# Kernel tuning notes

Measured on AMD Instinct MI355X. Metric: run time of the kernel, lower is better.

The kernel has to match this reference:

```python
import jax, jax.numpy as jnp
import numpy as np

N = 100_000      # nodes
E = 1_600_000    # edges (avg degree 16)
B = 50           # graphs in batch
GSIZE = N // B   # nodes per graph
IN = 128
HID = 128
NC = 10
K = 2


def setup_inputs() -> dict:
    key = jax.random.key(0)
    ks = jax.random.split(key, 10)
    # edges kept within each graph so the batched readout is realistic
    g = jax.random.randint(ks[0], (E,), 0, B)
    src = (g * GSIZE + jax.random.randint(ks[1], (E,), 0, GSIZE)).astype(jnp.int32)
    dst = (g * GSIZE + jax.random.randint(ks[2], (E,), 0, GSIZE)).astype(jnp.int32)
    graph_ids = (jnp.arange(N) // GSIZE).astype(jnp.int32)
    x = jax.random.normal(ks[3], (N, IN), jnp.float32)
    s1 = 1.0 / np.sqrt(K * IN)
    s2 = 1.0 / np.sqrt(K * HID)
    sc = 1.0 / np.sqrt(HID)
    W1 = jax.random.normal(ks[4], (K * IN, HID), jnp.float32) * s1
    b1 = jnp.zeros((HID,), jnp.float32)
    W2 = jax.random.normal(ks[5], (K * HID, HID), jnp.float32) * s2
    b2 = jnp.zeros((HID,), jnp.float32)
    Wc = jax.random.normal(ks[6], (HID, NC), jnp.float32) * sc
    bc = jnp.zeros((NC,), jnp.float32)
    return dict(x=x, W1=W1, b1=b1, W2=W2, b2=b2, Wc=Wc, bc=bc,
                src=src, dst=dst, graph_ids=graph_ids)


def _spmm_norm(feat, src, dst, dinv):
    # D^{-1/2} A D^{-1/2} feat  (copy_u + sum over in-edges)
    m = (feat * dinv)[src]                                    # [E, D]
    agg = jax.ops.segment_sum(m, dst, num_segments=N)         # [N, D]
    return agg * dinv


def _cheb_conv(feat, src, dst, dinv, W, b):
    # lambda_max = 2 -> re_norm = 1, L_hat = -D^{-1/2} A D^{-1/2}
    Tx0 = feat
    Tx1 = -_spmm_norm(feat, src, dst, dinv)                   # k=2 Cheb recursion
    h = jnp.concatenate([Tx0, Tx1], axis=-1) @ W + b          # DGL Linear(k*in, out)
    return jax.nn.relu(h)


def reference(x, W1, b1, W2, b2, Wc, bc, src, dst, graph_ids):
    deg = jax.ops.segment_sum(jnp.ones((E,), jnp.float32), dst, num_segments=N)
    dinv = jnp.clip(deg, 1.0, None) ** -0.5                   # in-degree^{-1/2}
    dinv = dinv[:, None]
    h = _cheb_conv(x, src, dst, dinv, W1, b1)                 # [N, HID]
    h = _cheb_conv(h, src, dst, dinv, W2, b2)                 # [N, HID]
    hg = jax.ops.segment_max(h, graph_ids, num_segments=B)    # MaxPooling readout [B, HID]
    return hg @ Wc + bc                                       # [B, NC]
```

## Files before the change

kernel.cpp:

```cpp
#include <hip/hip_runtime.h>

#define N_NODES 100000
#define N_EDGES 1600000
#define NB      50
#define GSIZE   2000
#define FEAT    128
#define NC      10
#define NSB     400
#define BCAP    5120
#define CHUNK   2048
#define NBLK_A  782

using short8 = __attribute__((ext_vector_type(8))) short;
using f32x4  = __attribute__((ext_vector_type(4))) float;

__device__ __forceinline__ unsigned bf16rnd(float f) {
    unsigned u = __float_as_uint(f);
    return (u + 0x7fffu + ((u >> 16) & 1u)) >> 16;
}
__device__ __forceinline__ float blo(unsigned w) { return __uint_as_float(w << 16); }
__device__ __forceinline__ float bhi(unsigned w) { return __uint_as_float(w & 0xffff0000u); }

__device__ __forceinline__ void gload_lds16(const void* g, void* l) {
    __builtin_amdgcn_global_load_lds(
        (const __attribute__((address_space(1))) unsigned int*)g,
        (__attribute__((address_space(3))) unsigned int*)l, 16, 0, 0);
}

__device__ __forceinline__ int graph_of(int k, int gi) {
    if (gi < 6) return k + 8 * gi;
    return (k < 2) ? (48 + k) : -1;
}

__global__ __launch_bounds__(256) void k_binA(
    const int* __restrict__ src, const int* __restrict__ dst,
    unsigned* __restrict__ gbuf, int* __restrict__ gcur) {
    __shared__ int cnt[NSB];
    __shared__ int base[NSB];
    __shared__ int gbase[NSB];
    __shared__ int tsum[256];
    __shared__ unsigned stage[CHUNK];
    __shared__ unsigned short bslot[CHUNK];
    __shared__ int total_s;
    int tid = threadIdx.x;
    int e0 = blockIdx.x * CHUNK;
    for (int i = tid; i < NSB; i += 256) cnt[i] = 0;
    __syncthreads();

    unsigned pv[8]; int pb[8], pr[8];
#pragma unroll
    for (int q = 0; q < 8; ++q) {
        int e = e0 + q * 256 + tid;
        pb[q] = -1;
        if (e < N_EDGES) {
            int d = dst[e];
            int g = d / 2000;
            int l = d - g * 2000;
            int sb = g * 8 + l / 250;
            pv[q] = ((unsigned)src[e] << 11) | (unsigned)l;
            pb[q] = sb;
            pr[q] = atomicAdd(&cnt[sb], 1);
        }
    }
    __syncthreads();
    int v0 = (2 * tid     < NSB) ? cnt[2 * tid]     : 0;
    int v1 = (2 * tid + 1 < NSB) ? cnt[2 * tid + 1] : 0;
    int loc = v0 + v1;
    tsum[tid] = loc; __syncthreads();
    for (int off = 1; off < 256; off <<= 1) {
        int t = (tid >= off) ? tsum[tid - off] : 0;
        __syncthreads(); tsum[tid] += t; __syncthreads();
    }
    int pref = tsum[tid] - loc;
    if (2 * tid     < NSB) base[2 * tid]     = pref;
    if (2 * tid + 1 < NSB) base[2 * tid + 1] = pref + v0;
    if (tid == 255) total_s = tsum[255];
    __syncthreads();
#pragma unroll
    for (int q = 0; q < 8; ++q) {
        if (pb[q] >= 0) {
            int s = base[pb[q]] + pr[q];
            stage[s] = pv[q];
            bslot[s] = (unsigned short)pb[q];
        }
    }
    for (int b = tid; b < NSB; b += 256) gbase[b] = atomicAdd(&gcur[b], cnt[b]);
    __syncthreads();
    int total = total_s;
    for (int s = tid; s < total; s += 256) {
        int b = bslot[s];
        gbuf[(size_t)b * BCAP + gbase[b] + (s - base[b])] = stage[s];
    }
}

__global__ __launch_bounds__(256) void k_prepB(
    const unsigned* __restrict__ gbuf, const int* __restrict__ gcur,
    int* __restrict__ rowstart, float* __restrict__ dinv, float* __restrict__ sdeg,
    int* __restrict__ csrc) {
    __shared__ int hist[256];
    __shared__ int tsum[256];
    __shared__ int lcur[256];
    __shared__ int stage[BCAP];
    __shared__ int base_s;
    int B = blockIdx.x; int k = B & 7, j = B >> 3;
    int gi = j >> 3, q = j & 7;
    int g = graph_of(k, gi);
    if (g < 0) return;
    int tid = threadIdx.x;
    int sb = g * 8 + q;
    int n0l = q * 250;
    hist[tid] = 0;
    int acc = 0;
    for (int i = tid; i < sb; i += 256) acc += gcur[i];
    tsum[tid] = acc;
    __syncthreads();
    for (int off = 128; off > 0; off >>= 1) {
        if (tid < off) tsum[tid] += tsum[tid + off];
        __syncthreads();
    }
    if (tid == 0) base_s = tsum[0];
    int nq = gcur[sb];
    const unsigned* bp = gbuf + (size_t)sb * BCAP;
    for (int i = tid; i < nq; i += 256)
        atomicAdd(&hist[(int)(bp[i] & 2047u) - n0l], 1);
    __syncthreads();
    int base = base_s;
    int v = hist[tid];
    tsum[tid] = v; __syncthreads();
    for (int off = 1; off < 256; off <<= 1) {
        int t = (tid >= off) ? tsum[tid - off] : 0;
        __syncthreads(); tsum[tid] += t; __syncthreads();
    }
    int pref = tsum[tid] - v;
    lcur[tid] = pref;
    if (tid < 250) {
        int node = g * GSIZE + n0l + tid;
        rowstart[node] = base + pref;
        float d = fmaxf((float)v, 1.f);
        dinv[node] = rsqrtf(d);
        sdeg[node] = sqrtf(d);
    }
    if (g == 49 && q == 7 && tid == 0) rowstart[N_NODES] = base + nq;
    __syncthreads();
    for (int i = tid; i < nq; i += 256) {
        unsigned w = bp[i];
        int d = (int)(w & 2047u) - n0l;
        int p = atomicAdd(&lcur[d], 1);
        stage[p] = (int)(w >> 11);
    }
    __syncthreads();
    for (int s = tid; s < nq; s += 256)
        csrc[base + s] = stage[s];
}

__global__ __launch_bounds__(256) void k_convert(const float* __restrict__ x,
                          const float* __restrict__ dinv, ushort* __restrict__ Yh) {
    int B = blockIdx.x; int k = B & 7, j = B >> 3;
    int gi = j / 250, local = j % 250;
    int g = graph_of(k, gi);
    if (g < 0) return;
    int tid = threadIdx.x;
    int r = tid >> 5, c = tid & 31;
    int node = g * GSIZE + local * 8 + r;
    float dv = dinv[node];
    float4 v = ((const float4*)x)[node * 32 + c];
    uint2 yo;
    yo.x = bf16rnd(v.x * dv) | (bf16rnd(v.y * dv) << 16);
    yo.y = bf16rnd(v.z * dv) | (bf16rnd(v.w * dv) << 16);
    ((uint2*)Yh)[node * 32 + c] = yo;
}

__global__ void k_packW(const float* __restrict__ W1, const float* __restrict__ W2,
                        ushort* __restrict__ W1h, ushort* __restrict__ W1l,
                        ushort* __restrict__ W2h, ushort* __restrict__ W2l) {
    int b = blockIdx.x;
    const float* W = (b < 128) ? W1 : W2;
    ushort* Wh = (b < 128) ? W1h : W2h;
    ushort* Wl = (b < 128) ? W1l : W2l;
    int idx = (b & 127) * 256 + threadIdx.x;
    int j = idx & 7, l = (idx >> 3) & 63, kb = (idx >> 9) & 7, c = idx >> 12;
    int k = kb * 32 + (l >> 4) * 8 + j;
    int col = c * 16 + (l & 15);
    float w = W[k * 128 + col];
    unsigned h = bf16rnd(w);
    float rem = w - __uint_as_float(h << 16);
    Wh[idx] = (ushort)h;
    Wl[idx] = (ushort)bf16rnd(rem);
}

__device__ __forceinline__ void acc8(float* a, uint4 u) {
    a[0] += blo(u.x); a[1] += bhi(u.x); a[2] += blo(u.y); a[3] += bhi(u.y);
    a[4] += blo(u.z); a[5] += bhi(u.z); a[6] += blo(u.w); a[7] += bhi(u.w);
}
__global__ __launch_bounds__(256) void k_gather(
    const ushort* __restrict__ Yh, const float* __restrict__ dinv,
    const int* __restrict__ rowstart, const int* __restrict__ csrc,
    ushort* __restrict__ Th) {
    int B = blockIdx.x; int k = B & 7, j = B >> 3;
    int gi = j / 125, local = j % 125;
    int g = graph_of(k, gi);
    if (g < 0) return;
    int tid = threadIdx.x;
    int c = tid & 15;
    int i = tid >> 4;
    int n = g * GSIZE + local * 16 + i;
    int rs = rowstart[n], re = rowstart[n + 1];
    const uint4* Y4 = (const uint4*)Yh;
    float a0[8] = {0.f}, a1[8] = {0.f}, a2[8] = {0.f}, a3[8] = {0.f};
    int e = rs;
    for (; e + 3 < re; e += 4) {
        int s0 = csrc[e], s1 = csrc[e + 1], s2 = csrc[e + 2], s3 = csrc[e + 3];
        uint4 u0 = Y4[s0 * 16 + c];
        uint4 u1 = Y4[s1 * 16 + c];
        uint4 u2 = Y4[s2 * 16 + c];
        uint4 u3 = Y4[s3 * 16 + c];
        acc8(a0, u0); acc8(a1, u1); acc8(a2, u2); acc8(a3, u3);
    }
    for (; e < re; ++e) {
        uint4 u = Y4[csrc[e] * 16 + c];
        acc8(a0, u);
    }
#pragma unroll
    for (int t = 0; t < 8; ++t) a0[t] = (a0[t] + a1[t]) + (a2[t] + a3[t]);
    float dn = -dinv[n];
    uint4 o;
    o.x = bf16rnd(a0[0] * dn) | (bf16rnd(a0[1] * dn) << 16);
    o.y = bf16rnd(a0[2] * dn) | (bf16rnd(a0[3] * dn) << 16);
    o.z = bf16rnd(a0[4] * dn) | (bf16rnd(a0[5] * dn) << 16);
    o.w = bf16rnd(a0[6] * dn) | (bf16rnd(a0[7] * dn) << 16);
    ((uint4*)Th)[n * 16 + c] = o;
}

__global__ __launch_bounds__(256, 4) void k_gemm(
    const ushort* __restrict__ Yh, const ushort* __restrict__ Th,
    const ushort* __restrict__ Wh, const ushort* __restrict__ Wl,
    const float* __restrict__ bias, const float* __restrict__ dinv,
    const float* __restrict__ sdeg,
    ushort* __restrict__ Oy, float* __restrict__ hg, int mode) {
    __shared__ uint4 ldsY[1280];
    __shared__ uint4 ldsT[1280];
    int B = blockIdx.x; int k = B & 7, j = B >> 3;
    int gi = j / 25, local = j % 25;
    int g = graph_of(k, gi);
    if (g < 0) return;
    int tid = threadIdx.x;
    int lane = tid & 63, wave = tid >> 6;
    int m = lane & 15, quad = lane >> 4;
    int rowbase = g * GSIZE + local * 80;

    const uint4* Y4 = (const uint4*)Yh;
    const uint4* T4 = (const uint4*)Th;
#pragma unroll
    for (int it = 0; it < 5; ++it) {
        int ci = it * 256 + tid;
        int lr = ci >> 4, cc = ci & 15;
        int sc = cc ^ (lr & 7);
        size_t go = (size_t)(rowbase + lr) * 16 + sc;
        uint4* ly = &ldsY[it * 256 + wave * 64];
        uint4* lt = &ldsT[it * 256 + wave * 64];
        gload_lds16(Y4 + go, ly);
        gload_lds16(T4 + go, lt);
    }
    __syncthreads();

#pragma unroll 1
    for (int ci2 = 0; ci2 < 2; ++ci2) {
        int c = wave + ci2 * 4;
        int colc = c * 16 + m;
        short8 wh[8], wl[8];
#pragma unroll
        for (int kb = 0; kb < 8; ++kb) {
            int bo = ((c * 8 + kb) * 64 + lane) * 8;
            wh[kb] = *reinterpret_cast<const short8*>(Wh + bo);
            wl[kb] = *reinterpret_cast<const short8*>(Wl + bo);
        }
#pragma unroll
        for (int kb = 0; kb < 8; ++kb) {
            asm volatile("" : "+v"(wh[kb]), "+v"(wl[kb]));
        }
        float bb = bias[colc];
        float runc = 0.f;

#pragma unroll 1
        for (int rt = 0; rt < 5; ++rt) {
            int wrow = rowbase + rt * 16;
            int lr = rt * 16 + m;
            f32x4 aA = {0.f, 0.f, 0.f, 0.f}, aB = {0.f, 0.f, 0.f, 0.f};
#pragma unroll
            for (int kb = 0; kb < 4; ++kb) {
                int qq = (kb * 4 + quad) ^ (m & 7);
                short8 aY = *reinterpret_cast<const short8*>(&ldsY[(lr << 4) | qq]);
                short8 aT = *reinterpret_cast<const short8*>(&ldsT[(lr << 4) | qq]);
                aA = __builtin_amdgcn_mfma_f32_16x16x32_bf16(aY, wh[kb],     aA, 0, 0, 0);
                aA = __builtin_amdgcn_mfma_f32_16x16x32_bf16(aY, wl[kb],     aA, 0, 0, 0);
                aB = __builtin_amdgcn_mfma_f32_16x16x32_bf16(aT, wh[kb + 4], aB, 0, 0, 0);
                aB = __builtin_amdgcn_mfma_f32_16x16x32_bf16(aT, wl[kb + 4], aB, 0, 0, 0);
            }
            if (mode == 0) {
#pragma unroll
                for (int r = 0; r < 4; ++r) {
                    int orow = wrow + quad * 4 + r;
                    float s = sdeg[orow], dv = dinv[orow];
                    float v = fmaxf(aA[r] * s + aB[r] + bb, 0.f);
                    Oy[orow * FEAT + colc] = (ushort)bf16rnd(v * dv);
                }
            } else {
#pragma unroll
                for (int r = 0; r < 4; ++r) {
                    float s = sdeg[wrow + quad * 4 + r];
                    runc = fmaxf(runc, fmaxf(aA[r] * s + aB[r] + bb, 0.f));
                }
            }
        }
        if (mode == 1) {
            runc = fmaxf(runc, __shfl_xor(runc, 16));
            runc = fmaxf(runc, __shfl_xor(runc, 32));
            if (lane < 16) {
                atomicMax((int*)&hg[g * FEAT + colc], __float_as_int(runc));
            }
        }
    }
}

__global__ void k_classify(const float* __restrict__ hg, const float* __restrict__ Wc,
                           const float* __restrict__ bc, float* __restrict__ out) {
    int g = blockIdx.x, t = threadIdx.x;
    if (t < NC) {
        float acc = bc[t];
        for (int j = 0; j < FEAT; ++j) acc += hg[g * FEAT + j] * Wc[j * NC + t];
        out[g * NC + t] = acc;
    }
}

extern "C" void kernel_launch(void* const* d_in, const int* in_sizes, int n_in,
                              void* d_out, int out_size, void* d_ws, size_t ws_size,
                              hipStream_t stream) {
    const float* x   = (const float*)d_in[0];
    const float* W1  = (const float*)d_in[1];
    const float* b1  = (const float*)d_in[2];
    const float* W2  = (const float*)d_in[3];
    const float* b2  = (const float*)d_in[4];
    const float* Wc  = (const float*)d_in[5];
    const float* bc  = (const float*)d_in[6];
    const int*   src = (const int*)d_in[7];
    const int*   dst = (const int*)d_in[8];
    float* out = (float*)d_out;

    char* ws = (char*)d_ws;
    size_t off = 0;
    auto alloc = [&](size_t bytes) { char* p = ws + off; off += (bytes + 255) & ~(size_t)255; return p; };
    int*      gcur     = (int*)     alloc(NSB * 4);
    float*    hg       = (float*)   alloc(NB * FEAT * 4);
    float*    dinv     = (float*)   alloc(N_NODES * 4);
    float*    sdeg     = (float*)   alloc(N_NODES * 4);
    int*      rowstart = (int*)     alloc((N_NODES + 1) * 4);
    unsigned* gbuf     = (unsigned*)alloc((size_t)NSB * BCAP * 4);
    int*      csrc     = (int*)     alloc((size_t)N_EDGES * 4);
    ushort*   W1h      = (ushort*)  alloc(256 * 128 * 2);
    ushort*   W1l      = (ushort*)  alloc(256 * 128 * 2);
    ushort*   W2h      = (ushort*)  alloc(256 * 128 * 2);
    ushort*   W2l      = (ushort*)  alloc(256 * 128 * 2);
    ushort*   Yh       = (ushort*)  alloc((size_t)N_NODES * FEAT * 2);
    ushort*   Y2h      = (ushort*)  alloc((size_t)N_NODES * FEAT * 2);
    ushort*   Th       = (ushort*)  alloc((size_t)N_NODES * FEAT * 2);

    hipMemsetAsync(gcur, 0, 1792 + NB * FEAT * 4, stream);

    k_binA<<<NBLK_A, 256, 0, stream>>>(src, dst, gbuf, gcur);
    k_prepB<<<448, 256, 0, stream>>>(gbuf, gcur, rowstart, dinv, sdeg, csrc);

    k_packW<<<256, 256, 0, stream>>>(W1, W2, W1h, W1l, W2h, W2l);
    k_convert<<<14000, 256, 0, stream>>>(x, dinv, Yh);

    k_gather<<<7000, 256, 0, stream>>>(Yh, dinv, rowstart, csrc, Th);
    k_gemm<<<1400, 256, 0, stream>>>(Yh, Th, W1h, W1l, b1, dinv, sdeg, Y2h, nullptr, 0);
    k_gather<<<7000, 256, 0, stream>>>(Y2h, dinv, rowstart, csrc, Th);
    k_gemm<<<1400, 256, 0, stream>>>(Y2h, Th, W2h, W2l, b2, dinv, sdeg, nullptr, hg, 1);

    k_classify<<<NB, 64, 0, stream>>>(hg, Wc, bc, out);
}
```

Baseline: 277.2 us.

## Fuse neighbor gather into GEMM kernel, keeping aggregated features in LDS

```diff
diff --git a/kernel.cpp b/kernel.cpp
--- a/kernel.cpp
+++ b/kernel.cpp
@@ -30,6 +30,11 @@
 __device__ __forceinline__ int graph_of(int k, int gi) {
     if (gi < 6) return k + 8 * gi;
     return (k < 2) ? (48 + k) : -1;
+}
+
+__device__ __forceinline__ void acc8(float* a, uint4 u) {
+    a[0] += blo(u.x); a[1] += bhi(u.x); a[2] += blo(u.y); a[3] += bhi(u.y);
+    a[4] += blo(u.z); a[5] += bhi(u.z); a[6] += blo(u.w); a[7] += bhi(u.w);
 }
 
 __global__ __launch_bounds__(256) void k_binA(
@@ -188,54 +193,12 @@
     Wl[idx] = (ushort)bf16rnd(rem);
 }
 
-__device__ __forceinline__ void acc8(float* a, uint4 u) {
-    a[0] += blo(u.x); a[1] += bhi(u.x); a[2] += blo(u.y); a[3] += bhi(u.y);
-    a[4] += blo(u.z); a[5] += bhi(u.z); a[6] += blo(u.w); a[7] += bhi(u.w);
-}
-__global__ __launch_bounds__(256) void k_gather(
-    const ushort* __restrict__ Yh, const float* __restrict__ dinv,
-    const int* __restrict__ rowstart, const int* __restrict__ csrc,
-    ushort* __restrict__ Th) {
-    int B = blockIdx.x; int k = B & 7, j = B >> 3;
-    int gi = j / 125, local = j % 125;
-    int g = graph_of(k, gi);
-    if (g < 0) return;
-    int tid = threadIdx.x;
-    int c = tid & 15;
-    int i = tid >> 4;
-    int n = g * GSIZE + local * 16 + i;
-    int rs = rowstart[n], re = rowstart[n + 1];
-    const uint4* Y4 = (const uint4*)Yh;
-    float a0[8] = {0.f}, a1[8] = {0.f}, a2[8] = {0.f}, a3[8] = {0.f};
-    int e = rs;
-    for (; e + 3 < re; e += 4) {
-        int s0 = csrc[e], s1 = csrc[e + 1], s2 = csrc[e + 2], s3 = csrc[e + 3];
-        uint4 u0 = Y4[s0 * 16 + c];
-        uint4 u1 = Y4[s1 * 16 + c];
-        uint4 u2 = Y4[s2 * 16 + c];
-        uint4 u3 = Y4[s3 * 16 + c];
-        acc8(a0, u0); acc8(a1, u1); acc8(a2, u2); acc8(a3, u3);
-    }
-    for (; e < re; ++e) {
-        uint4 u = Y4[csrc[e] * 16 + c];
-        acc8(a0, u);
-    }
-#pragma unroll
-    for (int t = 0; t < 8; ++t) a0[t] = (a0[t] + a1[t]) + (a2[t] + a3[t]);
-    float dn = -dinv[n];
-    uint4 o;
-    o.x = bf16rnd(a0[0] * dn) | (bf16rnd(a0[1] * dn) << 16);
-    o.y = bf16rnd(a0[2] * dn) | (bf16rnd(a0[3] * dn) << 16);
-    o.z = bf16rnd(a0[4] * dn) | (bf16rnd(a0[5] * dn) << 16);
-    o.w = bf16rnd(a0[6] * dn) | (bf16rnd(a0[7] * dn) << 16);
-    ((uint4*)Th)[n * 16 + c] = o;
-}
-
-__global__ __launch_bounds__(256, 4) void k_gemm(
-    const ushort* __restrict__ Yh, const ushort* __restrict__ Th,
+__global__ __launch_bounds__(256, 4) void k_gg(
+    const ushort* __restrict__ Yh,
     const ushort* __restrict__ Wh, const ushort* __restrict__ Wl,
     const float* __restrict__ bias, const float* __restrict__ dinv,
     const float* __restrict__ sdeg,
+    const int* __restrict__ rowstart, const int* __restrict__ csrc,
     ushort* __restrict__ Oy, float* __restrict__ hg, int mode) {
     __shared__ uint4 ldsY[1280];
     __shared__ uint4 ldsT[1280];
@@ -249,17 +212,47 @@
     int rowbase = g * GSIZE + local * 80;
 
     const uint4* Y4 = (const uint4*)Yh;
-    const uint4* T4 = (const uint4*)Th;
 #pragma unroll
     for (int it = 0; it < 5; ++it) {
         int ci = it * 256 + tid;
         int lr = ci >> 4, cc = ci & 15;
         int sc = cc ^ (lr & 7);
         size_t go = (size_t)(rowbase + lr) * 16 + sc;
-        uint4* ly = &ldsY[it * 256 + wave * 64];
-        uint4* lt = &ldsT[it * 256 + wave * 64];
-        gload_lds16(Y4 + go, ly);
-        gload_lds16(T4 + go, lt);
+        gload_lds16(Y4 + go, &ldsY[it * 256 + wave * 64]);
+    }
+
+    {
+        int c = tid & 15;
+        int i = tid >> 4;
+#pragma unroll 1
+        for (int b = 0; b < 5; ++b) {
+            int lr = b * 16 + i;
+            int n = rowbase + lr;
+            int rs = rowstart[n], re = rowstart[n + 1];
+            float a0[8] = {0.f}, a1[8] = {0.f}, a2[8] = {0.f}, a3[8] = {0.f};
+            int e = rs;
+            for (; e + 3 < re; e += 4) {
+                int s0 = csrc[e], s1 = csrc[e + 1], s2 = csrc[e + 2], s3 = csrc[e + 3];
+                uint4 u0 = Y4[s0 * 16 + c];
+                uint4 u1 = Y4[s1 * 16 + c];
+                uint4 u2 = Y4[s2 * 16 + c];
+                uint4 u3 = Y4[s3 * 16 + c];
+                acc8(a0, u0); acc8(a1, u1); acc8(a2, u2); acc8(a3, u3);
+            }
+            for (; e < re; ++e) {
+                uint4 u = Y4[csrc[e] * 16 + c];
+                acc8(a0, u);
+            }
+#pragma unroll
+            for (int t = 0; t < 8; ++t) a0[t] = (a0[t] + a1[t]) + (a2[t] + a3[t]);
+            float dn = -dinv[n];
+            uint4 o;
+            o.x = bf16rnd(a0[0] * dn) | (bf16rnd(a0[1] * dn) << 16);
+            o.y = bf16rnd(a0[2] * dn) | (bf16rnd(a0[3] * dn) << 16);
+            o.z = bf16rnd(a0[4] * dn) | (bf16rnd(a0[5] * dn) << 16);
+            o.w = bf16rnd(a0[6] * dn) | (bf16rnd(a0[7] * dn) << 16);
+            ldsT[(lr << 4) | (c ^ (i & 7))] = o;
+        }
     }
     __syncthreads();
 
@@ -362,7 +355,6 @@
     ushort*   W2l      = (ushort*)  alloc(256 * 128 * 2);
     ushort*   Yh       = (ushort*)  alloc((size_t)N_NODES * FEAT * 2);
     ushort*   Y2h      = (ushort*)  alloc((size_t)N_NODES * FEAT * 2);
-    ushort*   Th       = (ushort*)  alloc((size_t)N_NODES * FEAT * 2);
 
     hipMemsetAsync(gcur, 0, 1792 + NB * FEAT * 4, stream);
 
@@ -372,10 +364,8 @@
     k_packW<<<256, 256, 0, stream>>>(W1, W2, W1h, W1l, W2h, W2l);
     k_convert<<<14000, 256, 0, stream>>>(x, dinv, Yh);
 
-    k_gather<<<7000, 256, 0, stream>>>(Yh, dinv, rowstart, csrc, Th);
-    k_gemm<<<1400, 256, 0, stream>>>(Yh, Th, W1h, W1l, b1, dinv, sdeg, Y2h, nullptr, 0);
-    k_gather<<<7000, 256, 0, stream>>>(Y2h, dinv, rowstart, csrc, Th);
-    k_gemm<<<1400, 256, 0, stream>>>(Y2h, Th, W2h, W2l, b2, dinv, sdeg, nullptr, hg, 1);
+    k_gg<<<1400, 256, 0, stream>>>(Yh, W1h, W1l, b1, dinv, sdeg, rowstart, csrc, Y2h, nullptr, 0);
+    k_gg<<<1400, 256, 0, stream>>>(Y2h, W2h, W2l, b2, dinv, sdeg, rowstart, csrc, nullptr, hg, 1);
 
     k_classify<<<NB, 64, 0, stream>>>(hg, Wc, bc, out);
 }
```

After: 287.0 us. +3.5%, slower.
